# Performance work log

Measured on AMD Instinct MI355X. Metric: run time of the kernel, lower is better.

Reference implementation:

```python
import jax, jax.numpy as jnp
import numpy as np

B, T, IN = 4096, 64, 3
D, H, NB = 128, 4, 2
DH = D // H  # 32
EPS = 1e-5


def layer_norm(x, g, b):
    mu = x.mean(-1, keepdims=True)
    v = x.var(-1, keepdims=True)
    return (x - mu) / jnp.sqrt(v + EPS) * g + b


def group_norm(x, g, b):
    # headwise GroupNorm over the last dim split into H groups of DH
    xr = x.reshape(x.shape[:-1] + (H, DH))
    mu = xr.mean(-1, keepdims=True)
    v = xr.var(-1, keepdims=True)
    xn = ((xr - mu) / jnp.sqrt(v + EPS)).reshape(x.shape)
    return xn * g + b


def slstm(xg, R):
    # xg: [B,T,4,D] input-driven gate preactivations (i,f,z,o)
    # R : [4,H,DH,DH] block-diagonal (per-head) recurrent kernels per gate
    Bb = xg.shape[0]

    def step(carry, g):
        h, c, n, m = carry  # each [B,D]
        r = jnp.einsum('bhd,ghde->bghe', h.reshape(Bb, H, DH), R).reshape(Bb, 4, D)
        g = g + r
        it, ft, zt, ot = g[:, 0], g[:, 1], g[:, 2], g[:, 3]
        m_new = jnp.maximum(ft + m, it)          # stabilizer state
        i = jnp.exp(it - m_new)                  # stabilized exp input gate
        f = jnp.exp(ft + m - m_new)              # stabilized exp forget gate
        c_new = f * c + i * jnp.tanh(zt)
        n_new = f * n + i                        # normalizer state
        h_new = jax.nn.sigmoid(ot) * c_new / n_new
        return (h_new, c_new, n_new, m_new), h_new

    init = tuple(jnp.zeros((Bb, D), xg.dtype) for _ in range(4))
    _, hs = jax.lax.scan(step, init, jnp.swapaxes(xg, 0, 1))  # [T,B,D]
    return jnp.swapaxes(hs, 0, 1)


def setup_inputs() -> dict:
    key = jax.random.key(0)
    ks = jax.random.split(key, 12)
    s_in = 1.0 / np.sqrt(IN)
    s_d = 1.0 / np.sqrt(D)
    inp = {
        'x': jax.random.normal(ks[0], (B, T, IN), jnp.float32),
        'w_in': jax.random.normal(ks[1], (IN, D), jnp.float32) * s_in,
        'b_in': jnp.zeros((D,), jnp.float32),
        'ln1_g': jnp.ones((NB, D), jnp.float32),
        'ln1_b': jnp.zeros((NB, D), jnp.float32),
        'Wg': jax.random.normal(ks[2], (NB, D, 4 * D), jnp.float32) * s_d,
        'bg': jnp.zeros((NB, 4 * D), jnp.float32),
        'Rg': jax.random.normal(ks[3], (NB, 4, H, DH, DH), jnp.float32) / np.sqrt(DH),
        'gn_g': jnp.ones((NB, D), jnp.float32),
        'gn_b': jnp.zeros((NB, D), jnp.float32),
        'ln2_g': jnp.ones((NB, D), jnp.float32),
        'ln2_b': jnp.zeros((NB, D), jnp.float32),
        'W1': jax.random.normal(ks[4], (NB, D, D), jnp.float32) * s_d,
        'W2': jax.random.normal(ks[5], (NB, D, D), jnp.float32) * s_d,
        'lnf_g': jnp.ones((D,), jnp.float32),
        'lnf_b': jnp.zeros((D,), jnp.float32),
        'w_out': jax.random.normal(ks[6], (D, 1), jnp.float32) * s_d,
        'b_out': jnp.zeros((1,), jnp.float32),
    }
    return inp


def reference(x, w_in, b_in, ln1_g, ln1_b, Wg, bg, Rg, gn_g, gn_b,
              ln2_g, ln2_b, W1, W2, lnf_g, lnf_b, w_out, b_out):
    h = x @ w_in + b_in  # [B,T,D]
    for blk in range(NB):
        # sLSTM sub-block (pre-LN residual)
        xn = layer_norm(h, ln1_g[blk], ln1_b[blk])
        xg = (xn @ Wg[blk] + bg[blk]).reshape(h.shape[0], T, 4, D)
        hs = slstm(xg, Rg[blk])
        h = h + group_norm(hs, gn_g[blk], gn_b[blk])
        # FFN sub-block (pre-LN residual, proj_factor=1.0, gelu, no bias)
        yn = layer_norm(h, ln2_g[blk], ln2_b[blk])
        h = h + jax.nn.gelu(yn @ W1[blk]) @ W2[blk]
    h = layer_norm(h, lnf_g, lnf_b)  # post-blocks norm
    out = (h[:, -1, :] @ w_out + b_out)[:, 0]  # [B]
    return out
```

## Files before the change

### kernel.cpp

```cpp
#include <hip/hip_runtime.h>
#include <hip/hip_bf16.h>
#include <cstdint>
#include <cstddef>

#define EPS 1e-5f
#define BB 4096
#define TT 64
#define NBLK 2
#define MROWS (BB * TT)

typedef unsigned short ushort_t;
typedef __attribute__((ext_vector_type(8))) short short8;
typedef __attribute__((ext_vector_type(4))) float floatx4;

__device__ __forceinline__ ushort_t f2b(float f) {
    __hip_bfloat16 h = __float2bfloat16(f);
    return *reinterpret_cast<ushort_t*>(&h);
}
__device__ __forceinline__ float tanh_fast(float z) {
    return 1.f - 2.f / (__expf(2.f * z) + 1.f);
}
__device__ __forceinline__ float rcp_f(float x) {
    return __builtin_amdgcn_rcpf(x);
}
__device__ __forceinline__ void lds_barrier() {
    asm volatile("s_waitcnt lgkmcnt(0)\n\ts_barrier" ::: "memory");
}

template <int CTRL>
__device__ __forceinline__ float ror_add(float v) {
    int r = __builtin_amdgcn_update_dpp(
        0, __builtin_bit_cast(int, v), CTRL, 0xf, 0xf, false);
    return v + __builtin_bit_cast(float, r);
}
__device__ __forceinline__ float red16(float v) {
    v = ror_add<0x121>(v);
    v = ror_add<0x122>(v);
    v = ror_add<0x124>(v);
    v = ror_add<0x128>(v);
    return v;
}

__global__ __launch_bounds__(256) void k_cvtall(
    const float* __restrict__ Wg, const float* __restrict__ W1,
    const float* __restrict__ W2, ushort_t* __restrict__ Wgt,
    ushort_t* __restrict__ W1t, ushort_t* __restrict__ W2t) {
    int idx = blockIdx.x * 256 + threadIdx.x;
    if (idx < 2 * 512 * 128) {
        int blk = idx >> 16, r = idx & 65535;
        int k = r >> 9, n = r & 511;
        Wgt[(size_t)blk * 65536 + n * 128 + k] = f2b(Wg[idx]);
    } else if (idx < 2 * 512 * 128 + 2 * 128 * 128) {
        int i2 = idx - 2 * 512 * 128;
        int blk = i2 >> 14, r = i2 & 16383;
        int k = r >> 7, n = r & 127;
        W1t[(size_t)blk * 16384 + n * 128 + k] = f2b(W1[i2]);
    } else {
        int i2 = idx - (2 * 512 * 128 + 2 * 128 * 128);
        int blk = i2 >> 14, r = i2 & 16383;
        int k = r >> 7, n = r & 127;
        W2t[(size_t)blk * 16384 + n * 128 + k] = f2b(W2[i2]);
    }
}

template <bool EMBED, bool LASTONLY>
__global__ __launch_bounds__(512, 2) void k_gslstm(
    float* __restrict__ h, const float* __restrict__ x,
    const float* __restrict__ w_in, const float* __restrict__ b_in,
    const ushort_t* __restrict__ Wgt, const float* __restrict__ bg,
    const float* __restrict__ Rg,
    const float* __restrict__ ln1g, const float* __restrict__ ln1b,
    const float* __restrict__ gng, const float* __restrict__ gnb) {
    __shared__ float xg_ring[2][512][20];
    __shared__ float hin_ring[3][16][132];
    __shared__ ushort_t Afrag[2][16][136];
    __shared__ ushort_t tpose[4][16][40];

    const int tid = threadIdx.x;
    const int lane = tid & 63;
    const int wave = tid >> 6;
    const int q = lane >> 4;
    const int ml = lane & 15;
    const int b0 = blockIdx.x * 16;

    if (wave < 4) {
        const int p = wave;
        const int row = p * 4 + q;
        short8 WB[4][8];
#pragma unroll
        for (int ks = 0; ks < 4; ++ks)
#pragma unroll
            for (int s = 0; s < 8; ++s)
                WB[ks][s] = *(const short8*)(Wgt +
                    ((size_t)(p * 128 + s * 16 + ml) * 128 + ks * 32 + q * 8));
        float biasv[8];
#pragma unroll
        for (int s = 0; s < 8; ++s) biasv[s] = bg[p * 128 + s * 16 + ml];

        const float4 Lg0 = *(const float4*)(ln1g + ml * 8);
        const float4 Lg1 = *(const float4*)(ln1g + ml * 8 + 4);
        const float4 Lb0 = *(const float4*)(ln1b + ml * 8);
        const float4 Lb1 = *(const float4*)(ln1b + ml * 8 + 4);
        float4 W00{}, W01{}, W10{}, W11{}, W20{}, W21{}, BE0{}, BE1{};
        if (EMBED) {
            W00 = *(const float4*)(w_in + 0 * 128 + ml * 8);
            W01 = *(const float4*)(w_in + 0 * 128 + ml * 8 + 4);
            W10 = *(const float4*)(w_in + 1 * 128 + ml * 8);
            W11 = *(const float4*)(w_in + 1 * 128 + ml * 8 + 4);
            W20 = *(const float4*)(w_in + 2 * 128 + ml * 8);
            W21 = *(const float4*)(w_in + 2 * 128 + ml * 8 + 4);
            BE0 = *(const float4*)(b_in + ml * 8);
            BE1 = *(const float4*)(b_in + ml * 8 + 4);
        }

        auto issue_in = [&](int tt, float4& A, float4& B) {
            const float4* hp =
                (const float4*)(h + ((size_t)(b0 + row) * TT + tt) * 128 + ml * 8);
            A = hp[0]; B = hp[1];
        };
        auto issue_x = [&](int tt, float& x0, float& x1, float& x2) {
            const float* xp = x + ((size_t)(b0 + row) * TT + tt) * 3;
            x0 = xp[0]; x1 = xp[1]; x2 = xp[2];
        };
        auto embed_v = [&](float x0, float x1, float x2, float* v) {
            const float w0[8] = {W00.x, W00.y, W00.z, W00.w, W01.x, W01.y, W01.z, W01.w};
            const float w1[8] = {W10.x, W10.y, W10.z, W10.w, W11.x, W11.y, W11.z, W11.w};
            const float w2[8] = {W20.x, W20.y, W20.z, W20.w, W21.x, W21.y, W21.z, W21.w};
            const float be[8] = {BE0.x, BE0.y, BE0.z, BE0.w, BE1.x, BE1.y, BE1.z, BE1.w};
#pragma unroll
            for (int j = 0; j < 8; ++j)
                v[j] = x0 * w0[j] + x1 * w1[j] + x2 * w2[j] + be[j];
        };
        auto ln_stage = [&](const float* v, int aslot, int rslot) {
            float s = 0.f, ss = 0.f;
#pragma unroll
            for (int j = 0; j < 8; ++j) { s += v[j]; ss += v[j] * v[j]; }
            s = red16(s);
            ss = red16(ss);
            float mu = s * (1.f / 128.f);
            float rstd = rsqrtf(ss * (1.f / 128.f) - mu * mu + EPS);
            const float gg[8] = {Lg0.x, Lg0.y, Lg0.z, Lg0.w, Lg1.x, Lg1.y, Lg1.z, Lg1.w};
            const float bbv[8] = {Lb0.x, Lb0.y, Lb0.z, Lb0.w, Lb1.x, Lb1.y, Lb1.z, Lb1.w};
            ushort_t pk[8];
#pragma unroll
            for (int j = 0; j < 8; ++j)
                pk[j] = f2b((v[j] - mu) * rstd * gg[j] + bbv[j]);
            *(short8*)&Afrag[aslot][row][ml * 8] = *(const short8*)pk;
            *(float4*)&hin_ring[rslot][row][ml * 8] = *(const float4*)v;
            *(float4*)&hin_ring[rslot][row][ml * 8 + 4] = *(const float4*)(v + 4);
        };
        auto gemm_stage = [&](int slot) {
            short8 af[4];
#pragma unroll
            for (int ks = 0; ks < 4; ++ks)
                af[ks] = *(const short8*)&Afrag[slot][ml][ks * 32 + q * 8];
            floatx4 acc[8];
#pragma unroll
            for (int s = 0; s < 8; ++s) {
                float b = biasv[s];
                acc[s] = (floatx4){b, b, b, b};
            }
#pragma unroll
            for (int ks = 0; ks < 4; ++ks)
#pragma unroll
                for (int s = 0; s < 8; ++s)
                    acc[s] = __builtin_amdgcn_mfma_f32_16x16x32_bf16(
                        af[ks], WB[ks][s], acc[s], 0, 0, 0);
#pragma unroll
            for (int s = 0; s < 8; ++s)
                *(floatx4*)&xg_ring[slot][p * 128 + s * 16 + ml][q * 4] = acc[s];
        };

        float4 pA0, pA1, pB0, pB1;
        float px0 = 0.f, px1 = 0.f, px2 = 0.f, qx0 = 0.f, qx1 = 0.f, qx2 = 0.f;
        {
            float v[8];
            if (EMBED) {
                float a0, a1, a2, d0, d1, d2v;
                issue_x(0, a0, a1, a2);
                issue_x(1, d0, d1, d2v);
                issue_x(2, px0, px1, px2);
                embed_v(a0, a1, a2, v);  ln_stage(v, 0, 0);
                embed_v(d0, d1, d2v, v); ln_stage(v, 1, 1);
            } else {
                float4 a0, a1, d0, d1;
                issue_in(0, a0, a1);
                issue_in(1, d0, d1);
                issue_in(2, pA0, pA1);
                *(float4*)v = a0; *(float4*)(v + 4) = a1; ln_stage(v, 0, 0);
                *(float4*)v = d0; *(float4*)(v + 4) = d1; ln_stage(v, 1, 1);
            }
        }
        lds_barrier();
        gemm_stage(0);
        lds_barrier();

        int rs2 = 2, rs3 = 0;
#pragma unroll 1
        for (int t = 0; t < TT; t += 2) {
            if (t + 3 < TT) {
                if (EMBED) issue_x(t + 3, qx0, qx1, qx2);
                else       issue_in(t + 3, pB0, pB1);
            }
            gemm_stage((t + 1) & 1);
            if (t + 2 < TT) {
                float v[8];
                if (EMBED) embed_v(px0, px1, px2, v);
                else { *(float4*)v = pA0; *(float4*)(v + 4) = pA1; }
                ln_stage(v, t & 1, rs2);
            }
            lds_barrier();
            if (t + 4 < TT) {
                if (EMBED) issue_x(t + 4, px0, px1, px2);
                else       issue_in(t + 4, pA0, pA1);
            }
            if (t + 2 < TT) gemm_stage(t & 1);
            if (t + 3 < TT) {
                float v[8];
                if (EMBED) embed_v(qx0, qx1, qx2, v);
                else { *(float4*)v = pB0; *(float4*)(v + 4) = pB1; }
                ln_stage(v, (t + 1) & 1, rs3);
            }
            lds_barrier();
            rs2 += 2; if (rs2 >= 3) rs2 -= 3;
            rs3 += 2; if (rs3 >= 3) rs3 -= 3;
        }
    } else {
        __builtin_amdgcn_s_setprio(1);
        const int hd = wave - 4;
        short8 RB[4][2];
#pragma unroll
        for (int g = 0; g < 4; ++g)
#pragma unroll
            for (int d2 = 0; d2 < 2; ++d2) {
                ushort_t tmp[8];
#pragma unroll
                for (int j = 0; j < 8; ++j)
                    tmp[j] = f2b(Rg[(size_t)g * 4096 + hd * 1024 +
                                    (q * 8 + j) * 32 + d2 * 16 + ml]);
                RB[g][d2] = *(const short8*)tmp;
            }
        const float gng0 = gng[hd * 32 + ml], gng1 = gng[hd * 32 + 16 + ml];
        const float gnb0 = gnb[hd * 32 + ml], gnb1 = gnb[hd * 32 + 16 + ml];
        float cst[8], nst[8], mst[8];
#pragma unroll
        for (int i = 0; i < 8; ++i) { cst[i] = 0.f; nst[i] = 0.f; mst[i] = 0.f; }
        {
            ushort_t* tp = &tpose[hd][0][0];
            for (int i = lane; i < 16 * 40; i += 64) tp[i] = 0;
        }

        auto scan_iter = [&](int t, int rs) {
            short8 h8 = *(const short8*)&tpose[hd][ml][q * 8];
            floatx4 acc[4][2];
#pragma unroll
            for (int g = 0; g < 4; ++g)
#pragma unroll
                for (int d2 = 0; d2 < 2; ++d2)
                    acc[g][d2] = *(const floatx4*)
                        &xg_ring[t & 1][g * 128 + hd * 32 + d2 * 16 + ml][q * 4];
#pragma unroll
            for (int g = 0; g < 4; ++g)
#pragma unroll
                for (int d2 = 0; d2 < 2; ++d2)
                    acc[g][d2] = __builtin_amdgcn_mfma_f32_16x16x32_bf16(
                        h8, RB[g][d2], acc[g][d2], 0, 0, 0);
            float hv[2][4];
#pragma unroll
            for (int d2 = 0; d2 < 2; ++d2)
#pragma unroll
                for (int r = 0; r < 4; ++r) {
                    const int si = d2 * 4 + r;
                    float it = acc[0][d2][r], ft = acc[1][d2][r];
                    float zt = acc[2][d2][r], ot = acc[3][d2][r];
                    float mn = fmaxf(ft + mst[si], it);
                    float iv = __expf(it - mn);
                    float fv = __expf(ft + mst[si] - mn);
                    float e2 = __expf(2.f * zt);
                    float th = 1.f - 2.f * rcp_f(e2 + 1.f);
                    float cn = fv * cst[si] + iv * th;
                    float nn = fv * nst[si] + iv;
                    float eo = __expf(-ot);
                    hv[d2][r] = cn * rcp_f(nn + nn * eo);
                    cst[si] = cn; nst[si] = nn; mst[si] = mn;
                }
#pragma unroll
            for (int d2 = 0; d2 < 2; ++d2)
#pragma unroll
                for (int r = 0; r < 4; ++r)
                    tpose[hd][q * 4 + r][d2 * 16 + ml] = f2b(hv[d2][r]);
            if (!LASTONLY || t == TT - 1) {
                float hinv[4][2];
#pragma unroll
                for (int r = 0; r < 4; ++r)
#pragma unroll
                    for (int d2 = 0; d2 < 2; ++d2)
                        hinv[r][d2] =
                            hin_ring[rs][q * 4 + r][hd * 32 + d2 * 16 + ml];
                float s[4], ss[4];
#pragma unroll
                for (int r = 0; r < 4; ++r) {
                    s[r] = hv[0][r] + hv[1][r];
                    ss[r] = hv[0][r] * hv[0][r] + hv[1][r] * hv[1][r];
                }
#pragma unroll
                for (int r = 0; r < 4; ++r) {
                    s[r] = red16(s[r]);
                    ss[r] = red16(ss[r]);
                }
#pragma unroll
                for (int r = 0; r < 4; ++r) {
                    float mu = s[r] * (1.f / 32.f);
                    float rstd = rsqrtf(ss[r] * (1.f / 32.f) - mu * mu + EPS);
#pragma unroll
                    for (int d2 = 0; d2 < 2; ++d2) {
                        float gv = d2 ? gng1 : gng0;
                        float bv = d2 ? gnb1 : gnb0;
                        h[((size_t)(b0 + q * 4 + r) * TT + t) * 128 +
                          hd * 32 + d2 * 16 + ml] =
                            hinv[r][d2] + (hv[d2][r] - mu) * rstd * gv + bv;
                    }
                }
            }
        };

        lds_barrier();
        lds_barrier();
        int rs = 0;
#pragma unroll 1
        for (int t = 0; t < TT; t += 2) {
            scan_iter(t, rs);
            lds_barrier();
            scan_iter(t + 1, rs == 2 ? 0 : rs + 1);
            lds_barrier();
            rs += 2; if (rs >= 3) rs -= 3;
        }
    }
}

template <int NT>
__global__ __launch_bounds__(256, 3) void k_ffn_pipe(
    float* __restrict__ h, const ushort_t* __restrict__ W1t,
    const ushort_t* __restrict__ W2t,
    const float* __restrict__ lng, const float* __restrict__ lnb) {
    __shared__ float Hraw[32][132];
    __shared__ ushort_t T1[32][136];
    __shared__ __align__(16) char Ubuf[32 * 132 * 4];
    auto As = (ushort_t(*)[136])Ubuf;
    auto T2 = (float(*)[132])Ubuf;

    int tid = threadIdx.x;
    int lane = tid & 63, wave = tid >> 6;
    int q = lane >> 4, ml = lane & 15;
    int wn = wave * 32;
    int r = tid >> 3, qd = tid & 7;
    int hi = lane >> 5, lo = lane & 31;
    size_t base = (size_t)blockIdx.x * (32 * NT);

    short8 W1B[2][4];
#pragma unroll
    for (int jn = 0; jn < 2; ++jn)
#pragma unroll
        for (int ks = 0; ks < 4; ++ks)
            W1B[jn][ks] = *(const short8*)(W1t +
                ((size_t)(wn + jn * 16 + ml) * 128 + ks * 32 + q * 8));

    float4 cur[4], nxt[4];
#pragma unroll
    for (int k = 0; k < 4; ++k)
        cur[k] = *(const float4*)(h + (base + wave * 8 + 2 * k + hi) * 128 + lo * 4);

#pragma unroll 1
    for (int it = 0; it < NT; ++it) {
#pragma unroll
        for (int k = 0; k < 4; ++k)
            *(float4*)&Hraw[wave * 8 + 2 * k + hi][lo * 4] = cur[k];
        if (it + 1 < NT) {
#pragma unroll
            for (int k = 0; k < 4; ++k)
                nxt[k] = *(const float4*)(h +
                    (base + (it + 1) * 32 + wave * 8 + 2 * k + hi) * 128 + lo * 4);
        }
        lds_barrier();

        float4 hv[4];
#pragma unroll
        for (int k = 0; k < 4; ++k)
            hv[k] = *(const float4*)&Hraw[r][qd * 16 + k * 4];
        float s = 0.f, ss = 0.f;
#pragma unroll
        for (int k = 0; k < 4; ++k) {
            float4 v = hv[k];
            s += v.x + v.y + v.z + v.w;
            ss += v.x * v.x + v.y * v.y + v.z * v.z + v.w * v.w;
        }
        s += __shfl_xor(s, 1); ss += __shfl_xor(ss, 1);
        s += __shfl_xor(s, 2); ss += __shfl_xor(ss, 2);
        s += __shfl_xor(s, 4); ss += __shfl_xor(ss, 4);
        float mu = s * (1.f / 128.f);
        float rstd = rsqrtf(ss * (1.f / 128.f) - mu * mu + EPS);
#pragma unroll
        for (int kk = 0; kk < 2; ++kk) {
            float4 a = hv[2 * kk];
            float4 b = hv[2 * kk + 1];
            int c0 = qd * 16 + kk * 8;
            float4 g0 = *(const float4*)(lng + c0);
            float4 g1 = *(const float4*)(lng + c0 + 4);
            float4 b0 = *(const float4*)(lnb + c0);
            float4 b1 = *(const float4*)(lnb + c0 + 4);
            ushort_t p[8];
            p[0] = f2b((a.x - mu) * rstd * g0.x + b0.x);
            p[1] = f2b((a.y - mu) * rstd * g0.y + b0.y);
            p[2] = f2b((a.z - mu) * rstd * g0.z + b0.z);
            p[3] = f2b((a.w - mu) * rstd * g0.w + b0.w);
            p[4] = f2b((b.x - mu) * rstd * g1.x + b1.x);
            p[5] = f2b((b.y - mu) * rstd * g1.y + b1.y);
            p[6] = f2b((b.z - mu) * rstd * g1.z + b1.z);
            p[7] = f2b((b.w - mu) * rstd * g1.w + b1.w);
            *(short8*)&As[r][c0] = *(const short8*)p;
        }
        lds_barrier();

        floatx4 acc[2][2];
#pragma unroll
        for (int i = 0; i < 2; ++i)
#pragma unroll
            for (int j = 0; j < 2; ++j) acc[i][j] = (floatx4)0.f;
#pragma unroll
        for (int ks = 0; ks < 4; ++ks) {
            short8 af[2];
#pragma unroll
            for (int im = 0; im < 2; ++im)
                af[im] = *(const short8*)&As[im * 16 + ml][ks * 32 + q * 8];
#pragma unroll
            for (int im = 0; im < 2; ++im)
#pragma unroll
                for (int jn = 0; jn < 2; ++jn)
                    acc[im][jn] = __builtin_amdgcn_mfma_f32_16x16x32_bf16(
                        af[im], W1B[jn][ks], acc[im][jn], 0, 0, 0);
        }
#pragma unroll
        for (int im = 0; im < 2; ++im)
#pragma unroll
            for (int jn = 0; jn < 2; ++jn)
#pragma unroll
                for (int rr = 0; rr < 4; ++rr) {
                    float v = acc[im][jn][rr];
                    float u = 0.7978845608028654f * (v + 0.044715f * v * v * v);
                    float gv = 0.5f * v * (1.f + tanh_fast(u));
                    T1[im * 16 + q * 4 + rr][wn + jn * 16 + ml] = f2b(gv);
                }
        short8 W2B[2][4];
#pragma unroll
        for (int jn = 0; jn < 2; ++jn)
#pragma unroll
            for (int ks = 0; ks < 4; ++ks)
                W2B[jn][ks] = *(const short8*)(W2t +
                    ((size_t)(wn + jn * 16 + ml) * 128 + ks * 32 + q * 8));
        lds_barrier();

#pragma unroll
        for (int i = 0; i < 2; ++i)
#pragma unroll
            for (int j = 0; j < 2; ++j) acc[i][j] = (floatx4)0.f;
#pragma unroll
        for (int ks = 0; ks < 4; ++ks) {
            short8 af[2];
#pragma unroll
            for (int im = 0; im < 2; ++im)
                af[im] = *(const short8*)&T1[im * 16 + ml][ks * 32 + q * 8];
#pragma unroll
            for (int im = 0; im < 2; ++im)
#pragma unroll
                for (int jn = 0; jn < 2; ++jn)
                    acc[im][jn] = __builtin_amdgcn_mfma_f32_16x16x32_bf16(
                        af[im], W2B[jn][ks], acc[im][jn], 0, 0, 0);
        }
#pragma unroll
        for (int im = 0; im < 2; ++im)
#pragma unroll
            for (int jn = 0; jn < 2; ++jn)
#pragma unroll
                for (int rr = 0; rr < 4; ++rr)
                    T2[im * 16 + q * 4 + rr][wn + jn * 16 + ml] = acc[im][jn][rr];
        lds_barrier();

#pragma unroll
        for (int k = 0; k < 4; ++k) {
            float4 t2v = *(const float4*)&T2[wave * 8 + 2 * k + hi][lo * 4];
            float4 o;
            o.x = cur[k].x + t2v.x;
            o.y = cur[k].y + t2v.y;
            o.z = cur[k].z + t2v.z;
            o.w = cur[k].w + t2v.w;
            *(float4*)(h + (base + it * 32 + wave * 8 + 2 * k + hi) * 128 + lo * 4) = o;
        }
        if (it + 1 < NT) {
#pragma unroll
            for (int k = 0; k < 4; ++k) cur[k] = nxt[k];
        }
    }
}

__global__ __launch_bounds__(256, 6) void k_tail(
    const float* __restrict__ h, const ushort_t* __restrict__ W1t,
    const ushort_t* __restrict__ W2t,
    const float* __restrict__ lng, const float* __restrict__ lnb,
    const float* __restrict__ lnfg, const float* __restrict__ lnfb,
    const float* __restrict__ w_out, const float* __restrict__ b_out,
    float* __restrict__ out) {
    __shared__ __align__(16) char U[32 * 136 * 2 * 2];
    auto As = (ushort_t(*)[136])U;
    auto T1 = (ushort_t(*)[136])(U + 32 * 136 * 2);
    auto F = (float(*)[136])U;
    int tid = threadIdx.x;
    int lane = tid & 63, wave = tid >> 6;
    int q = lane >> 4, ml = lane & 15;
    int wn = wave * 32;
    size_t row0 = (size_t)blockIdx.x * 32;

    short8 W1B[2][4];
#pragma unroll
    for (int jn = 0; jn < 2; ++jn)
#pragma unroll
        for (int ks = 0; ks < 4; ++ks)
            W1B[jn][ks] = *(const short8*)(W1t +
                ((size_t)(wn + jn * 16 + ml) * 128 + ks * 32 + q * 8));

    int r = tid >> 3, qd = tid & 7;
    size_t grow = (row0 + r) * TT + (TT - 1);
    const float* hrow = h + grow * 128 + qd * 16;
    float s = 0.f, ss = 0.f;
#pragma unroll
    for (int k = 0; k < 4; ++k) {
        float4 v = ((const float4*)hrow)[k];
        s += v.x + v.y + v.z + v.w;
        ss += v.x * v.x + v.y * v.y + v.z * v.z + v.w * v.w;
    }
    s += __shfl_xor(s, 1); ss += __shfl_xor(ss, 1);
    s += __shfl_xor(s, 2); ss += __shfl_xor(ss, 2);
    s += __shfl_xor(s, 4); ss += __shfl_xor(ss, 4);
    float mu = s * (1.f / 128.f);
    float rstd = rsqrtf(ss * (1.f / 128.f) - mu * mu + EPS);
#pragma unroll
    for (int kk = 0; kk < 2; ++kk) {
        float4 a = ((const float4*)hrow)[2 * kk];
        float4 b = ((const float4*)hrow)[2 * kk + 1];
        int c0 = qd * 16 + kk * 8;
        float4 g0 = *(const float4*)(lng + c0);
        float4 g1 = *(const float4*)(lng + c0 + 4);
        float4 b0 = *(const float4*)(lnb + c0);
        float4 b1 = *(const float4*)(lnb + c0 + 4);
        ushort_t p[8];
        p[0] = f2b((a.x - mu) * rstd * g0.x + b0.x);
        p[1] = f2b((a.y - mu) * rstd * g0.y + b0.y);
        p[2] = f2b((a.z - mu) * rstd * g0.z + b0.z);
        p[3] = f2b((a.w - mu) * rstd * g0.w + b0.w);
        p[4] = f2b((b.x - mu) * rstd * g1.x + b1.x);
        p[5] = f2b((b.y - mu) * rstd * g1.y + b1.y);
        p[6] = f2b((b.z - mu) * rstd * g1.z + b1.z);
        p[7] = f2b((b.w - mu) * rstd * g1.w + b1.w);
        *(short8*)&As[r][c0] = *(const short8*)p;
    }
    lds_barrier();

    floatx4 acc[2][2];
#pragma unroll
    for (int i = 0; i < 2; ++i)
#pragma unroll
        for (int j = 0; j < 2; ++j) acc[i][j] = (floatx4)0.f;
#pragma unroll
    for (int ks = 0; ks < 4; ++ks) {
        short8 af[2];
#pragma unroll
        for (int im = 0; im < 2; ++im)
            af[im] = *(const short8*)&As[im * 16 + ml][ks * 32 + q * 8];
#pragma unroll
        for (int im = 0; im < 2; ++im)
#pragma unroll
            for (int jn = 0; jn < 2; ++jn)
                acc[im][jn] = __builtin_amdgcn_mfma_f32_16x16x32_bf16(
                    af[im], W1B[jn][ks], acc[im][jn], 0, 0, 0);
    }
#pragma unroll
    for (int im = 0; im < 2; ++im)
#pragma unroll
        for (int jn = 0; jn < 2; ++jn)
#pragma unroll
            for (int rr = 0; rr < 4; ++rr) {
                float v = acc[im][jn][rr];
                float u = 0.7978845608028654f * (v + 0.044715f * v * v * v);
                float gv = 0.5f * v * (1.f + tanh_fast(u));
                T1[im * 16 + q * 4 + rr][wn + jn * 16 + ml] = f2b(gv);
            }
    short8 W2B[2][4];
#pragma unroll
    for (int jn = 0; jn < 2; ++jn)
#pragma unroll
        for (int ks = 0; ks < 4; ++ks)
            W2B[jn][ks] = *(const short8*)(W2t +
                ((size_t)(wn + jn * 16 + ml) * 128 + ks * 32 + q * 8));
    lds_barrier();

    float rres[2][2][4];
#pragma unroll
    for (int im = 0; im < 2; ++im)
#pragma unroll
        for (int jn = 0; jn < 2; ++jn)
#pragma unroll
            for (int rr = 0; rr < 4; ++rr) {
                int rloc = im * 16 + q * 4 + rr;
                rres[im][jn][rr] = h[((row0 + rloc) * TT + (TT - 1)) * 128 +
                                     wn + jn * 16 + ml];
            }
#pragma unroll
    for (int i = 0; i < 2; ++i)
#pragma unroll
        for (int j = 0; j < 2; ++j) acc[i][j] = (floatx4)0.f;
#pragma unroll
    for (int ks = 0; ks < 4; ++ks) {
        short8 af[2];
#pragma unroll
        for (int im = 0; im < 2; ++im)
            af[im] = *(const short8*)&T1[im * 16 + ml][ks * 32 + q * 8];
#pragma unroll
        for (int im = 0; im < 2; ++im)
#pragma unroll
            for (int jn = 0; jn < 2; ++jn)
                acc[im][jn] = __builtin_amdgcn_mfma_f32_16x16x32_bf16(
                    af[im], W2B[jn][ks], acc[im][jn], 0, 0, 0);
    }
    lds_barrier();
#pragma unroll
    for (int im = 0; im < 2; ++im)
#pragma unroll
        for (int jn = 0; jn < 2; ++jn)
#pragma unroll
            for (int rr = 0; rr < 4; ++rr) {
                int rloc = im * 16 + q * 4 + rr;
                F[rloc][wn + jn * 16 + ml] = rres[im][jn][rr] + acc[im][jn][rr];
            }
    lds_barrier();

    float4 fv[4];
#pragma unroll
    for (int k = 0; k < 4; ++k)
        fv[k] = *(const float4*)&F[r][qd * 16 + k * 4];
    float s2 = 0.f, ss2 = 0.f;
#pragma unroll
    for (int k = 0; k < 4; ++k) {
        float4 v = fv[k];
        s2 += v.x + v.y + v.z + v.w;
        ss2 += v.x * v.x + v.y * v.y + v.z * v.z + v.w * v.w;
    }
    s2 += __shfl_xor(s2, 1); ss2 += __shfl_xor(ss2, 1);
    s2 += __shfl_xor(s2, 2); ss2 += __shfl_xor(ss2, 2);
    s2 += __shfl_xor(s2, 4); ss2 += __shfl_xor(ss2, 4);
    float mu2 = s2 * (1.f / 128.f);
    float rstd2 = rsqrtf(ss2 * (1.f / 128.f) - mu2 * mu2 + EPS);
    float dot = 0.f;
#pragma unroll
    for (int k = 0; k < 4; ++k) {
        int c0 = qd * 16 + k * 4;
        float4 g = *(const float4*)(lnfg + c0);
        float4 bb = *(const float4*)(lnfb + c0);
        float4 w = *(const float4*)(w_out + c0);
        dot += ((fv[k].x - mu2) * rstd2 * g.x + bb.x) * w.x +
               ((fv[k].y - mu2) * rstd2 * g.y + bb.y) * w.y +
               ((fv[k].z - mu2) * rstd2 * g.z + bb.z) * w.z +
               ((fv[k].w - mu2) * rstd2 * g.w + bb.w) * w.w;
    }
    dot += __shfl_xor(dot, 1);
    dot += __shfl_xor(dot, 2);
    dot += __shfl_xor(dot, 4);
    if (qd == 0) out[row0 + r] = dot + b_out[0];
}

extern "C" void kernel_launch(void* const* d_in, const int* in_sizes, int n_in,
                              void* d_out, int out_size, void* d_ws, size_t ws_size,
                              hipStream_t stream) {
    const float* x    = (const float*)d_in[0];
    const float* w_in = (const float*)d_in[1];
    const float* b_in = (const float*)d_in[2];
    const float* ln1g = (const float*)d_in[3];
    const float* ln1b = (const float*)d_in[4];
    const float* Wg   = (const float*)d_in[5];
    const float* bg   = (const float*)d_in[6];
    const float* Rg   = (const float*)d_in[7];
    const float* gng  = (const float*)d_in[8];
    const float* gnb  = (const float*)d_in[9];
    const float* ln2g = (const float*)d_in[10];
    const float* ln2b = (const float*)d_in[11];
    const float* W1   = (const float*)d_in[12];
    const float* W2   = (const float*)d_in[13];
    const float* lnfg = (const float*)d_in[14];
    const float* lnfb = (const float*)d_in[15];
    const float* wout = (const float*)d_in[16];
    const float* bout = (const float*)d_in[17];
    float* out = (float*)d_out;

    float* h = (float*)d_ws;
    ushort_t* Wgt = (ushort_t*)(h + (size_t)MROWS * 128);
    ushort_t* W1t = Wgt + 2 * 512 * 128;
    ushort_t* W2t = W1t + 2 * 128 * 128;

    k_cvtall<<<(2 * 512 * 128 + 4 * 128 * 128) / 256, 256, 0, stream>>>(
        Wg, W1, W2, Wgt, W1t, W2t);

    k_gslstm<true, false><<<BB / 16, 512, 0, stream>>>(
        h, x, w_in, b_in, Wgt, bg, Rg, ln1g, ln1b, gng, gnb);
    k_ffn_pipe<8><<<MROWS / 256, 256, 0, stream>>>(h, W1t, W2t, ln2g, ln2b);
    k_gslstm<false, true><<<BB / 16, 512, 0, stream>>>(
        h, nullptr, nullptr, nullptr, Wgt + (size_t)512 * 128, bg + 512,
        Rg + (size_t)16384, ln1g + 128, ln1b + 128, gng + 128, gnb + 128);
    k_tail<<<BB / 32, 256, 0, stream>>>(h, W1t + 16384, W2t + 16384,
                                        ln2g + 128, ln2b + 128,
                                        lnfg, lnfb, wout, bout, out);
}
```

Measured before the change: 353.6 us.

## Drop hin_ring LDS buffer, reload residual in scan waves, raise occupancy

Removes the shared-memory residual ring by having the scan waves reload the residual input straight from global memory, or recompute the embedding from x when EMBED is set. The gate ring's padding shrinks from 20 to 16 columns, and an XOR-style column swizzle keeps bank conflicts down. Together these cut LDS use so launch bounds can request 4 blocks per SM instead of 2, giving more overlap across blocks. The cost is extra global loads on the latency-critical scan path and tighter register limits, which could cause spills.

```diff
diff --git a/kernel.cpp b/kernel.cpp
--- a/kernel.cpp
+++ b/kernel.cpp
@@ -64,15 +64,14 @@
 }
 
 template <bool EMBED, bool LASTONLY>
-__global__ __launch_bounds__(512, 2) void k_gslstm(
+__global__ __launch_bounds__(512, 4) void k_gslstm(
     float* __restrict__ h, const float* __restrict__ x,
     const float* __restrict__ w_in, const float* __restrict__ b_in,
     const ushort_t* __restrict__ Wgt, const float* __restrict__ bg,
     const float* __restrict__ Rg,
     const float* __restrict__ ln1g, const float* __restrict__ ln1b,
     const float* __restrict__ gng, const float* __restrict__ gnb) {
-    __shared__ float xg_ring[2][512][20];
-    __shared__ float hin_ring[3][16][132];
+    __shared__ float xg_ring[2][512][16];
     __shared__ ushort_t Afrag[2][16][136];
     __shared__ ushort_t tpose[4][16][40];
 
@@ -82,6 +81,7 @@
     const int q = lane >> 4;
     const int ml = lane & 15;
     const int b0 = blockIdx.x * 16;
+    const int xc = ((q + (ml >> 1)) & 3) * 4;
 
     if (wave < 4) {
         const int p = wave;
@@ -131,7 +131,7 @@
             for (int j = 0; j < 8; ++j)
                 v[j] = x0 * w0[j] + x1 * w1[j] + x2 * w2[j] + be[j];
         };
-        auto ln_stage = [&](const float* v, int aslot, int rslot) {
+        auto ln_stage = [&](const float* v, int aslot) {
             float s = 0.f, ss = 0.f;
 #pragma unroll
             for (int j = 0; j < 8; ++j) { s += v[j]; ss += v[j] * v[j]; }
@@ -146,8 +146,6 @@
             for (int j = 0; j < 8; ++j)
                 pk[j] = f2b((v[j] - mu) * rstd * gg[j] + bbv[j]);
             *(short8*)&Afrag[aslot][row][ml * 8] = *(const short8*)pk;
-            *(float4*)&hin_ring[rslot][row][ml * 8] = *(const float4*)v;
-            *(float4*)&hin_ring[rslot][row][ml * 8 + 4] = *(const float4*)(v + 4);
         };
         auto gemm_stage = [&](int slot) {
             short8 af[4];
@@ -168,7 +166,7 @@
                         af[ks], WB[ks][s], acc[s], 0, 0, 0);
 #pragma unroll
             for (int s = 0; s < 8; ++s)
-                *(floatx4*)&xg_ring[slot][p * 128 + s * 16 + ml][q * 4] = acc[s];
+                *(floatx4*)&xg_ring[slot][p * 128 + s * 16 + ml][xc] = acc[s];
         };
 
         float4 pA0, pA1, pB0, pB1;
@@ -180,22 +178,21 @@
                 issue_x(0, a0, a1, a2);
                 issue_x(1, d0, d1, d2v);
                 issue_x(2, px0, px1, px2);
-                embed_v(a0, a1, a2, v);  ln_stage(v, 0, 0);
-                embed_v(d0, d1, d2v, v); ln_stage(v, 1, 1);
+                embed_v(a0, a1, a2, v);  ln_stage(v, 0);
+                embed_v(d0, d1, d2v, v); ln_stage(v, 1);
             } else {
                 float4 a0, a1, d0, d1;
                 issue_in(0, a0, a1);
                 issue_in(1, d0, d1);
                 issue_in(2, pA0, pA1);
-                *(float4*)v = a0; *(float4*)(v + 4) = a1; ln_stage(v, 0, 0);
-                *(float4*)v = d0; *(float4*)(v + 4) = d1; ln_stage(v, 1, 1);
+                *(float4*)v = a0; *(float4*)(v + 4) = a1; ln_stage(v, 0);
+                *(float4*)v = d0; *(float4*)(v + 4) = d1; ln_stage(v, 1);
             }
         }
         lds_barrier();
         gemm_stage(0);
         lds_barrier();
 
-        int rs2 = 2, rs3 = 0;
 #pragma unroll 1
         for (int t = 0; t < TT; t += 2) {
             if (t + 3 < TT) {
@@ -207,7 +204,7 @@
                 float v[8];
                 if (EMBED) embed_v(px0, px1, px2, v);
                 else { *(float4*)v = pA0; *(float4*)(v + 4) = pA1; }
-                ln_stage(v, t & 1, rs2);
+                ln_stage(v, t & 1);
             }
             lds_barrier();
             if (t + 4 < TT) {
@@ -219,11 +216,9 @@
                 float v[8];
                 if (EMBED) embed_v(qx0, qx1, qx2, v);
                 else { *(float4*)v = pB0; *(float4*)(v + 4) = pB1; }
-                ln_stage(v, (t + 1) & 1, rs3);
+                ln_stage(v, (t + 1) & 1);
             }
             lds_barrier();
-            rs2 += 2; if (rs2 >= 3) rs2 -= 3;
-            rs3 += 2; if (rs3 >= 3) rs3 -= 3;
         }
     } else {
         __builtin_amdgcn_s_setprio(1);
@@ -242,6 +237,16 @@
             }
         const float gng0 = gng[hd * 32 + ml], gng1 = gng[hd * 32 + 16 + ml];
         const float gnb0 = gnb[hd * 32 + ml], gnb1 = gnb[hd * 32 + 16 + ml];
+        float we[3][2], beh[2];
+        if (EMBED) {
+#pragma unroll
+            for (int d2 = 0; d2 < 2; ++d2) {
+#pragma unroll
+                for (int c = 0; c < 3; ++c)
+                    we[c][d2] = w_in[c * 128 + hd * 32 + d2 * 16 + ml];
+                beh[d2] = b_in[hd * 32 + d2 * 16 + ml];
+            }
+        }
         float cst[8], nst[8], mst[8];
 #pragma unroll
         for (int i = 0; i < 8; ++i) { cst[i] = 0.f; nst[i] = 0.f; mst[i] = 0.f; }
@@ -250,7 +255,27 @@
             for (int i = lane; i < 16 * 40; i += 64) tp[i] = 0;
         }
 
-        auto scan_iter = [&](int t, int rs) {
+        auto scan_iter = [&](int t) {
+            const bool doGN = (!LASTONLY || t == TT - 1);
+            float xv[4][3];
+            float hg[4][2];
+            if (doGN) {
+                if (EMBED) {
+#pragma unroll
+                    for (int r = 0; r < 4; ++r) {
+                        const float* xp =
+                            x + ((size_t)(b0 + q * 4 + r) * TT + t) * 3;
+                        xv[r][0] = xp[0]; xv[r][1] = xp[1]; xv[r][2] = xp[2];
+                    }
+                } else {
+#pragma unroll
+                    for (int r = 0; r < 4; ++r)
+#pragma unroll
+                        for (int d2 = 0; d2 < 2; ++d2)
+                            hg[r][d2] = h[((size_t)(b0 + q * 4 + r) * TT + t) * 128 +
+                                          hd * 32 + d2 * 16 + ml];
+                }
+            }
             short8 h8 = *(const short8*)&tpose[hd][ml][q * 8];
             floatx4 acc[4][2];
 #pragma unroll
@@ -258,7 +283,7 @@
 #pragma unroll
                 for (int d2 = 0; d2 < 2; ++d2)
                     acc[g][d2] = *(const floatx4*)
-                        &xg_ring[t & 1][g * 128 + hd * 32 + d2 * 16 + ml][q * 4];
+                        &xg_ring[t & 1][g * 128 + hd * 32 + d2 * 16 + ml][xc];
 #pragma unroll
             for (int g = 0; g < 4; ++g)
 #pragma unroll
@@ -289,14 +314,19 @@
 #pragma unroll
                 for (int r = 0; r < 4; ++r)
                     tpose[hd][q * 4 + r][d2 * 16 + ml] = f2b(hv[d2][r]);
-            if (!LASTONLY || t == TT - 1) {
+            if (doGN) {
                 float hinv[4][2];
 #pragma unroll
                 for (int r = 0; r < 4; ++r)
 #pragma unroll
-                    for (int d2 = 0; d2 < 2; ++d2)
-                        hinv[r][d2] =
-                            hin_ring[rs][q * 4 + r][hd * 32 + d2 * 16 + ml];
+                    for (int d2 = 0; d2 < 2; ++d2) {
+                        if (EMBED)
+                            hinv[r][d2] = xv[r][0] * we[0][d2] +
+                                          xv[r][1] * we[1][d2] +
+                                          xv[r][2] * we[2][d2] + beh[d2];
+                        else
+                            hinv[r][d2] = hg[r][d2];
+                    }
                 float s[4], ss[4];
 #pragma unroll
                 for (int r = 0; r < 4; ++r) {
@@ -326,14 +356,12 @@
 
         lds_barrier();
         lds_barrier();
-        int rs = 0;
 #pragma unroll 1
         for (int t = 0; t < TT; t += 2) {
-            scan_iter(t, rs);
+            scan_iter(t);
             lds_barrier();
-            scan_iter(t + 1, rs == 2 ? 0 : rs + 1);
+            scan_iter(t + 1);
             lds_barrier();
-            rs += 2; if (rs >= 3) rs -= 3;
         }
     }
 }
```

New measurement: 1.029 ms. +190.9%, slower.
